# Kernel tuning notes

Measured on AMD Instinct MI355X. Metric: run time of the kernel, lower is better.

Reference implementation:

```python
import jax, jax.numpy as jnp
import numpy as np

B, T, D_IN, D_OUT = 4, 2048, 1024, 1024


def setup_inputs() -> dict:
    key = jax.random.key(0)
    k1, k2, k3, k4 = jax.random.split(key, 4)
    s_in = 1.0 / np.sqrt(D_IN)
    return {
        "input_vector": jax.random.normal(k1, (B, T, D_IN), dtype=jnp.float32),
        "w_q": jax.random.normal(k2, (D_IN, D_OUT), dtype=jnp.float32) * s_in,
        "w_k": jax.random.normal(k3, (D_IN, D_OUT), dtype=jnp.float32) * s_in,
        "w_v": jax.random.normal(k4, (D_IN, D_OUT), dtype=jnp.float32) * s_in,
    }


def reference(input_vector, w_q, w_k, w_v):
    # projections: [B, T, D_OUT]
    q = jnp.einsum("btd,de->bte", input_vector, w_q)
    k = jnp.einsum("btd,de->bte", input_vector, w_k)
    v = jnp.einsum("btd,de->bte", input_vector, w_v)

    T_ = q.shape[1]
    # raw scores [B, T, T]
    scores = jnp.einsum("bqd,bkd->bqk", q, k)
    # causal mask (strict upper triangle masked to -inf), applied BEFORE scaling
    # (as in the original; -inf is invariant under the scale anyway)
    causal = jnp.tril(jnp.ones((T_, T_), dtype=bool))  # True = keep
    scores = jnp.where(causal[None, :, :], scores, -jnp.inf)
    scores = scores / jnp.sqrt(jnp.asarray(k.shape[-1], scores.dtype))
    attn = jax.nn.softmax(scores, axis=-1)
    # dropout = 0.0 (eval): identity
    return jnp.einsum("bqk,bkd->bqd", attn, v)
```

## Files before the change

### kernel.cpp

```cpp
#include <hip/hip_runtime.h>
#include <cstdint>
#include <math.h>

typedef unsigned short u16;
typedef __attribute__((ext_vector_type(8))) short short8;
typedef __attribute__((ext_vector_type(16))) float f32x16;

__device__ __forceinline__ u16 f2bf(float f) {
  uint32_t u = __float_as_uint(f);
  u += 0x7FFFu + ((u >> 16) & 1u);
  return (u16)(u >> 16);
}
__device__ __forceinline__ float bf2f(u16 h) {
  return __uint_as_float(((uint32_t)h) << 16);
}

__device__ __forceinline__ void async_ld16(u16* lds, const u16* g) {
  __builtin_amdgcn_global_load_lds((const __attribute__((address_space(1))) uint32_t*)g,
                                   (__attribute__((address_space(3))) uint32_t*)lds,
                                   16, 0, 0);
}

template <int MODE, bool KLIM, int EPI>
__global__ __launch_bounds__(256) void gemm_bt(
    const u16* __restrict__ A, int lda, long zsA,
    const u16* __restrict__ B, int ldb, long zsB,
    void* __restrict__ Cv, int ldc, long zsC,
    float* __restrict__ l, int K, float scale, int NB)
{
  const int b = blockIdx.x, zb = blockIdx.y;
  int nb, mb;
  if constexpr (MODE == 1) {
    const int u = b & 7, v = b >> 3;
    nb = v & (NB - 1);
    mb = u * ((int)(gridDim.x >> 3) / NB) + (v / NB);
  } else if constexpr (MODE == 2) {
    const int u = b & 7, idx = b >> 3;
    if (idx <= u) { mb = u;      nb = idx; }
    else          { mb = 15 - u; nb = idx - u - 1; }
  } else if constexpr (MODE == 3) {
    const int u = b & 7, idx = b >> 3;
    mb = (idx < 8) ? u : 15 - u;
    nb = idx & 7;
  } else {
    nb = b % NB;
    mb = b / NB;
  }

  A += (long)zb * zsA;
  B += (long)zb * zsB;
  const int m0 = mb * 128, n0 = nb * 128;

  __shared__ __align__(16) u16 lsA[2][128 * 32];
  __shared__ __align__(16) u16 lsB[2][128 * 32];

  const int tid = threadIdx.x;
  const int lane = tid & 63;
  const int wave = tid >> 6;
  const int wr = (wave >> 1) * 64;
  const int wc = (wave & 1) * 64;

  f32x16 acc[2][2];
#pragma unroll
  for (int i = 0; i < 2; ++i)
#pragma unroll
    for (int j = 0; j < 2; ++j)
#pragma unroll
      for (int r = 0; r < 16; ++r) acc[i][j][r] = 0.f;

  const int c0 = tid;
  const int c1 = tid + 256;
  const int r0 = c0 >> 2, q0 = ((c0 & 3) ^ ((c0 >> 3) & 3)) * 8;
  const int r1 = c1 >> 2, q1 = ((c1 & 3) ^ ((c1 >> 3) & 3)) * 8;

  const int klim = (mb + 1) * 128;
  const int kmax = KLIM ? (K < klim ? K : klim) : K;

  const u16* pA0 = A + (long)(m0 + r0) * lda + q0;
  const u16* pA1 = A + (long)(m0 + r1) * lda + q1;
  const u16* pB0 = B + (long)(n0 + r0) * ldb + q0;
  const u16* pB1 = B + (long)(n0 + r1) * ldb + q1;

  const int m32 = lane & 31;
  const int hh = lane >> 5;
  const int rsw = (m32 >> 1) & 3;
  int offA[2][2], offB[2][2];
#pragma unroll
  for (int i = 0; i < 2; ++i)
#pragma unroll
    for (int ks = 0; ks < 2; ++ks) {
      const int kq = ((ks << 1) | hh) ^ rsw;
      offA[i][ks] = (wr + i * 32 + m32) * 32 + kq * 8;
      offB[i][ks] = (wc + i * 32 + m32) * 32 + kq * 8;
    }

  async_ld16(&lsA[0][c0 * 8], pA0);
  async_ld16(&lsA[0][c1 * 8], pA1);
  async_ld16(&lsB[0][c0 * 8], pB0);
  async_ld16(&lsB[0][c1 * 8], pB1);
  pA0 += 32; pA1 += 32; pB0 += 32; pB1 += 32;

  int p = 0;
  for (int k0 = 0; k0 < kmax; k0 += 32) {
    __syncthreads();
    if (k0 + 32 < kmax) {
      async_ld16(&lsA[p ^ 1][c0 * 8], pA0);
      async_ld16(&lsA[p ^ 1][c1 * 8], pA1);
      async_ld16(&lsB[p ^ 1][c0 * 8], pB0);
      async_ld16(&lsB[p ^ 1][c1 * 8], pB1);
      pA0 += 32; pA1 += 32; pB0 += 32; pB1 += 32;
    }

    const u16* la = lsA[p];
    const u16* lb = lsB[p];
#pragma unroll
    for (int ks = 0; ks < 2; ++ks) {
      const short8 a0 = *(const short8*)&la[offA[0][ks]];
      const short8 a1 = *(const short8*)&la[offA[1][ks]];
      const short8 b0 = *(const short8*)&lb[offB[0][ks]];
      const short8 b1 = *(const short8*)&lb[offB[1][ks]];
      acc[0][0] = __builtin_amdgcn_mfma_f32_32x32x16_bf16(a0, b0, acc[0][0], 0, 0, 0);
      acc[0][1] = __builtin_amdgcn_mfma_f32_32x32x16_bf16(a0, b1, acc[0][1], 0, 0, 0);
      acc[1][0] = __builtin_amdgcn_mfma_f32_32x32x16_bf16(a1, b0, acc[1][0], 0, 0, 0);
      acc[1][1] = __builtin_amdgcn_mfma_f32_32x32x16_bf16(a1, b1, acc[1][1], 0, 0, 0);
    }
    p ^= 1;
  }

  const int ec = lane & 31;
  const int rb = (lane >> 5) * 4;

  if constexpr (EPI == 1) {
    u16* C = (u16*)Cv + (long)zb * zsC;
#pragma unroll
    for (int i = 0; i < 2; ++i) {
      const int rbase = m0 + wr + i * 32 + rb;
#pragma unroll
      for (int j = 0; j < 2; ++j) {
        const int col = n0 + wc + j * 32 + ec;
#pragma unroll
        for (int r = 0; r < 16; ++r) {
          const int row = rbase + (r & 3) + 8 * (r >> 2);
          C[(long)row * ldc + col] = f2bf(acc[i][j][r] * scale);
        }
      }
    }
  } else if constexpr (EPI == 2) {
    u16* C = (u16*)Cv + (long)zb * zsC;
    float* lz = l + (long)zb * 2048;
#pragma unroll
    for (int i = 0; i < 2; ++i) {
      const int rbase = m0 + wr + i * 32 + rb;
      float rsum[16];
#pragma unroll
      for (int r = 0; r < 16; ++r) rsum[r] = 0.f;
#pragma unroll
      for (int j = 0; j < 2; ++j) {
        const int col = n0 + wc + j * 32 + ec;
#pragma unroll
        for (int r = 0; r < 16; ++r) {
          const int row = rbase + (r & 3) + 8 * (r >> 2);
          float pv = __expf(acc[i][j][r] * scale);
          if (col > row) pv = 0.f;
          C[(long)row * ldc + col] = f2bf(pv);
          rsum[r] += pv;
        }
      }
#pragma unroll
      for (int r = 0; r < 16; ++r) {
        float s = rsum[r];
#pragma unroll
        for (int off = 1; off < 32; off <<= 1) s += __shfl_xor(s, off, 64);
        if ((lane & 31) == 0)
          atomicAdd(&lz[rbase + (r & 3) + 8 * (r >> 2)], s);
      }
    }
  } else {
    float* C = (float*)Cv + (long)zb * zsC;
    const float* lz = l + (long)zb * 2048;
#pragma unroll
    for (int i = 0; i < 2; ++i) {
      const int rbase = m0 + wr + i * 32 + rb;
#pragma unroll
      for (int j = 0; j < 2; ++j) {
        const int col = n0 + wc + j * 32 + ec;
#pragma unroll
        for (int r = 0; r < 16; ++r) {
          const int row = rbase + (r & 3) + 8 * (r >> 2);
          C[(long)row * ldc + col] = acc[i][j][r] / lz[row];
        }
      }
    }
  }
}

__global__ __launch_bounds__(256) void cast_x_kernel(const float* __restrict__ x,
                                                     u16* __restrict__ y,
                                                     float* __restrict__ l) {
  const long i = ((long)blockIdx.x * 256 + threadIdx.x) * 4;
  const float4 v = *(const float4*)(x + i);
  ushort4 o;
  o.x = f2bf(v.x); o.y = f2bf(v.y); o.z = f2bf(v.z); o.w = f2bf(v.w);
  *(ushort4*)(y + i) = o;
  if (blockIdx.x == 0) {
    float4 z = {0.f, 0.f, 0.f, 0.f};
#pragma unroll
    for (int k = 0; k < 8; ++k)
      ((float4*)l)[threadIdx.x * 8 + k] = z;
  }
}

__global__ __launch_bounds__(256) void cast_wt_kernel(const float* __restrict__ w0,
                                                      const float* __restrict__ w1,
                                                      const float* __restrict__ w2,
                                                      u16* __restrict__ Wt) {
  const float* W = (blockIdx.z == 0) ? w0 : (blockIdx.z == 1) ? w1 : w2;
  u16* o = Wt + (long)blockIdx.z * 1024 * 1024;
  __shared__ float t[32][33];
  const int n0 = blockIdx.x * 32, k0 = blockIdx.y * 32;
  const int tx = threadIdx.x, ty = threadIdx.y;
  for (int r = ty; r < 32; r += 8) t[r][tx] = W[(long)(k0 + r) * 1024 + n0 + tx];
  __syncthreads();
  for (int r = ty; r < 32; r += 8) o[(long)(n0 + r) * 1024 + k0 + tx] = f2bf(t[tx][r]);
}

__global__ __launch_bounds__(256) void transpose_v_kernel(const u16* __restrict__ V,
                                                          u16* __restrict__ Vt) {
  __shared__ u16 t[32][33];
  const int d0 = blockIdx.x * 32, t0 = blockIdx.y * 32, b = blockIdx.z;
  const u16* Vb = V + (long)b * 2048 * 1024;
  u16* Ob = Vt + (long)b * 1024 * 2048;
  const int tx = threadIdx.x, ty = threadIdx.y;
  for (int r = ty; r < 32; r += 8) t[r][tx] = Vb[(long)(t0 + r) * 1024 + d0 + tx];
  __syncthreads();
  for (int r = ty; r < 32; r += 8) Ob[(long)(d0 + r) * 2048 + t0 + tx] = t[tx][r];
}

extern "C" void kernel_launch(void* const* d_in, const int* in_sizes, int n_in,
                              void* d_out, int out_size, void* d_ws, size_t ws_size,
                              hipStream_t stream) {
  const float* X  = (const float*)d_in[0];
  const float* Wq = (const float*)d_in[1];
  const float* Wk = (const float*)d_in[2];
  const float* Wv = (const float*)d_in[3];
  float* out = (float*)d_out;

  const long BT = 8192;
  const long Tq = 2048, D = 1024;

  u16* Xbf = (u16*)d_ws;
  u16* Wt  = Xbf + BT * D;
  u16* QKV = Wt + 3 * D * D;
  u16* Vt  = QKV + 3 * BT * D;
  u16* P   = Vt + 4 * D * Tq;
  float* l = (float*)(P + 4 * Tq * Tq);

  cast_x_kernel<<<8192, 256, 0, stream>>>(X, Xbf, l);
  cast_wt_kernel<<<dim3(32, 32, 3), dim3(32, 8), 0, stream>>>(Wq, Wk, Wv, Wt);

  gemm_bt<1, false, 1><<<dim3(512, 3), 256, 0, stream>>>(
      Xbf, 1024, 0L, Wt, 1024, D * D, QKV, 1024, BT * D, nullptr, 1024, 1.0f, 8);

  gemm_bt<2, false, 2><<<dim3(136, 4), 256, 0, stream>>>(
      QKV, 1024, Tq * D, QKV + BT * D, 1024, Tq * D,
      P, 2048, Tq * Tq, l, 1024, 0.03125f, 16);

  transpose_v_kernel<<<dim3(32, 64, 4), dim3(32, 8), 0, stream>>>(QKV + 2 * BT * D, Vt);

  gemm_bt<3, true, 3><<<dim3(128, 4), 256, 0, stream>>>(
      P, 2048, Tq * Tq, Vt, 2048, D * Tq,
      out, 1024, Tq * D, l, 2048, 1.0f, 8);
}
```

Baseline: 283.6 us.

## Compute V transposed directly, fuse scores with V projection, replace atomics with partials

The V projection now runs as Wv^T·X^T, so V is produced already transposed and the separate transpose kernel goes away. That projection is also merged into the same launch as the causal score/exp kernel. Row sums are written as per-column-block partials instead of atomicAdds, which also removes the zeroing of l. The PV kernel reduces those partials into shared memory before normalizing. The two cast kernels are merged into one launch, for fewer launches and less memory traffic overall, at the cost of a more complex role-dispatch kernel and strided Vt writes.

```diff
diff --git a/kernel.cpp b/kernel.cpp
--- a/kernel.cpp
+++ b/kernel.cpp
@@ -1,6 +1,5 @@
 #include <hip/hip_runtime.h>
 #include <cstdint>
-#include <math.h>
 
 typedef unsigned short u16;
 typedef __attribute__((ext_vector_type(8))) short short8;
@@ -11,9 +10,6 @@
   u += 0x7FFFu + ((u >> 16) & 1u);
   return (u16)(u >> 16);
 }
-__device__ __forceinline__ float bf2f(u16 h) {
-  return __uint_as_float(((uint32_t)h) << 16);
-}
 
 __device__ __forceinline__ void async_ld16(u16* lds, const u16* g) {
   __builtin_amdgcn_global_load_lds((const __attribute__((address_space(1))) uint32_t*)g,
@@ -21,98 +17,119 @@
                                    16, 0, 0);
 }
 
-template <int MODE, bool KLIM, int EPI>
-__global__ __launch_bounds__(256) void gemm_bt(
-    const u16* __restrict__ A, int lda, long zsA,
-    const u16* __restrict__ B, int ldb, long zsB,
-    void* __restrict__ Cv, int ldc, long zsC,
-    float* __restrict__ l, int K, float scale, int NB)
+template <int ROLE>
+__global__ __launch_bounds__(256) void gk(
+    const u16* __restrict__ Xbf, const u16* __restrict__ Wt,
+    u16* __restrict__ QK, u16* __restrict__ VtAll,
+    u16* __restrict__ P, float* __restrict__ lpart,
+    float* __restrict__ out)
 {
-  const int b = blockIdx.x, zb = blockIdx.y;
-  int nb, mb;
-  if constexpr (MODE == 1) {
-    const int u = b & 7, v = b >> 3;
-    nb = v & (NB - 1);
-    mb = u * ((int)(gridDim.x >> 3) / NB) + (v / NB);
-  } else if constexpr (MODE == 2) {
-    const int u = b & 7, idx = b >> 3;
-    if (idx <= u) { mb = u;      nb = idx; }
-    else          { mb = 15 - u; nb = idx - u - 1; }
-  } else if constexpr (MODE == 3) {
-    const int u = b & 7, idx = b >> 3;
-    mb = (idx < 8) ? u : 15 - u;
-    nb = idx & 7;
-  } else {
-    nb = b % NB;
-    mb = b / NB;
-  }
-
-  A += (long)zb * zsA;
-  B += (long)zb * zsB;
-  const int m0 = mb * 128, n0 = nb * 128;
-
-  __shared__ __align__(16) u16 lsA[2][128 * 32];
-  __shared__ __align__(16) u16 lsB[2][128 * 32];
-
+  const int b = blockIdx.x;
   const int tid = threadIdx.x;
   const int lane = tid & 63;
   const int wave = tid >> 6;
   const int wr = (wave >> 1) * 64;
   const int wc = (wave & 1) * 64;
 
-  f32x16 acc[2][2];
-#pragma unroll
-  for (int i = 0; i < 2; ++i)
-#pragma unroll
-    for (int j = 0; j < 2; ++j)
-#pragma unroll
-      for (int r = 0; r < 16; ++r) acc[i][j][r] = 0.f;
-
-  const int c0 = tid;
-  const int c1 = tid + 256;
+  __shared__ __align__(16) u16 ls[4][4096];
+  __shared__ float l_s[128];
+
+  const int c0 = tid, c1 = tid + 256;
   const int r0 = c0 >> 2, q0 = ((c0 & 3) ^ ((c0 >> 3) & 3)) * 8;
   const int r1 = c1 >> 2, q1 = ((c1 & 3) ^ ((c1 >> 3) & 3)) * 8;
 
-  const int klim = (mb + 1) * 128;
-  const int kmax = KLIM ? (K < klim ? K : klim) : K;
+  const int m32 = lane & 31;
+  const int hh = lane >> 5;
+  const int rsw = (m32 >> 1) & 3;
+  int offA[2][2], offB[2][2];
+#pragma unroll
+  for (int i = 0; i < 2; ++i)
+#pragma unroll
+    for (int ks = 0; ks < 2; ++ks) {
+      const int kq = ((ks << 1) | hh) ^ rsw;
+      offA[i][ks] = (wr + i * 32 + m32) * 32 + kq * 8;
+      offB[i][ks] = (wc + i * 32 + m32) * 32 + kq * 8;
+    }
+
+  const u16 *A, *B;
+  int lda, ldb, kmax, m0, n0, mb, nb, zb = 0, mat = 0;
+  bool scoresRole = false;
+
+  if constexpr (ROLE == 0) {
+    const int u = b & 7, v = b >> 3;
+    mat = v >> 6;
+    const int w = v & 63;
+    nb = w & 7;
+    mb = u * 8 + (w >> 3);
+    A = Xbf; lda = 1024;
+    B = Wt + (long)mat * 1024 * 1024; ldb = 1024;
+    kmax = 1024;
+  } else if constexpr (ROLE == 1) {
+    if (b < 544) {
+      scoresRole = true;
+      const int u = b & 7, t = b >> 3;
+      zb = t / 17;
+      const int idx = t % 17;
+      if (idx <= u) { mb = u;      nb = idx; }
+      else          { mb = 15 - u; nb = idx - u - 1; }
+      A = QK + (long)zb * 2048 * 1024; lda = 1024;
+      B = QK + 8192L * 1024 + (long)zb * 2048 * 1024; ldb = 1024;
+      kmax = 1024;
+    } else {
+      const int v = b - 544;
+      const int u = v & 7, w = v >> 3;
+      mb = w & 7;
+      nb = u * 8 + (w >> 3);
+      A = Wt + 2L * 1024 * 1024; lda = 1024;
+      B = Xbf; ldb = 1024;
+      kmax = 1024;
+    }
+  } else {
+    const int u = b & 7, idx = b >> 3;
+    zb = blockIdx.y;
+    if (idx < 8) { mb = 15 - u; nb = idx; }
+    else         { mb = u;      nb = idx - 8; }
+    A = P + (long)zb * 2048 * 2048; lda = 2048;
+    B = VtAll + (long)zb * 2048; ldb = 8192;
+    kmax = (mb + 1) * 128;
+  }
+  m0 = mb * 128;
+  n0 = nb * 128;
 
   const u16* pA0 = A + (long)(m0 + r0) * lda + q0;
   const u16* pA1 = A + (long)(m0 + r1) * lda + q1;
   const u16* pB0 = B + (long)(n0 + r0) * ldb + q0;
   const u16* pB1 = B + (long)(n0 + r1) * ldb + q1;
 
-  const int m32 = lane & 31;
-  const int hh = lane >> 5;
-  const int rsw = (m32 >> 1) & 3;
-  int offA[2][2], offB[2][2];
+  f32x16 acc[2][2];
 #pragma unroll
   for (int i = 0; i < 2; ++i)
 #pragma unroll
-    for (int ks = 0; ks < 2; ++ks) {
-      const int kq = ((ks << 1) | hh) ^ rsw;
-      offA[i][ks] = (wr + i * 32 + m32) * 32 + kq * 8;
-      offB[i][ks] = (wc + i * 32 + m32) * 32 + kq * 8;
-    }
-
-  async_ld16(&lsA[0][c0 * 8], pA0);
-  async_ld16(&lsA[0][c1 * 8], pA1);
-  async_ld16(&lsB[0][c0 * 8], pB0);
-  async_ld16(&lsB[0][c1 * 8], pB1);
+    for (int j = 0; j < 2; ++j)
+#pragma unroll
+      for (int r = 0; r < 16; ++r) acc[i][j][r] = 0.f;
+
+  async_ld16(&ls[0][c0 * 8 - 0], pA0);
+  async_ld16(&ls[0][c1 * 8 - 2048 * 0], pA1);
+  async_ld16(&ls[2][c0 * 8], pB0);
+  async_ld16(&ls[2][c1 * 8 - 2048 * 0], pB1);
   pA0 += 32; pA1 += 32; pB0 += 32; pB1 += 32;
 
   int p = 0;
   for (int k0 = 0; k0 < kmax; k0 += 32) {
     __syncthreads();
     if (k0 + 32 < kmax) {
-      async_ld16(&lsA[p ^ 1][c0 * 8], pA0);
-      async_ld16(&lsA[p ^ 1][c1 * 8], pA1);
-      async_ld16(&lsB[p ^ 1][c0 * 8], pB0);
-      async_ld16(&lsB[p ^ 1][c1 * 8], pB1);
+      u16* la = ls[p ^ 1];
+      u16* lb = ls[2 + (p ^ 1)];
+      async_ld16(&la[c0 * 8], pA0);
+      async_ld16(&la[c1 * 8], pA1);
+      async_ld16(&lb[c0 * 8], pB0);
+      async_ld16(&lb[c1 * 8], pB1);
       pA0 += 32; pA1 += 32; pB0 += 32; pB1 += 32;
     }
 
-    const u16* la = lsA[p];
-    const u16* lb = lsB[p];
+    const u16* la = ls[p];
+    const u16* lb = ls[2 + p];
 #pragma unroll
     for (int ks = 0; ks < 2; ++ks) {
       const short8 a0 = *(const short8*)&la[offA[0][ks]];
@@ -130,8 +147,8 @@
   const int ec = lane & 31;
   const int rb = (lane >> 5) * 4;
 
-  if constexpr (EPI == 1) {
-    u16* C = (u16*)Cv + (long)zb * zsC;
+  if constexpr (ROLE == 0) {
+    u16* C = QK + (long)mat * 8192 * 1024;
 #pragma unroll
     for (int i = 0; i < 2; ++i) {
       const int rbase = m0 + wr + i * 32 + rb;
@@ -141,99 +158,110 @@
 #pragma unroll
         for (int r = 0; r < 16; ++r) {
           const int row = rbase + (r & 3) + 8 * (r >> 2);
-          C[(long)row * ldc + col] = f2bf(acc[i][j][r] * scale);
-        }
-      }
-    }
-  } else if constexpr (EPI == 2) {
-    u16* C = (u16*)Cv + (long)zb * zsC;
-    float* lz = l + (long)zb * 2048;
+          C[(long)row * 1024 + col] = f2bf(acc[i][j][r]);
+        }
+      }
+    }
+  } else if constexpr (ROLE == 1) {
+    if (scoresRole) {
+      u16* C = P + (long)zb * 2048 * 2048;
+      float* lp = lpart + (long)zb * 32 * 2048 + (long)(2 * nb + (wc >> 6)) * 2048;
+#pragma unroll
+      for (int i = 0; i < 2; ++i) {
+        const int rbl = wr + i * 32 + rb;
+        float rsum[16];
+#pragma unroll
+        for (int r = 0; r < 16; ++r) rsum[r] = 0.f;
+#pragma unroll
+        for (int j = 0; j < 2; ++j) {
+          const int col = n0 + wc + j * 32 + ec;
+#pragma unroll
+          for (int r = 0; r < 16; ++r) {
+            const int row = m0 + rbl + (r & 3) + 8 * (r >> 2);
+            float pv = __expf(acc[i][j][r] * 0.03125f);
+            if (col > row) pv = 0.f;
+            C[(long)row * 2048 + col] = f2bf(pv);
+            rsum[r] += pv;
+          }
+        }
+#pragma unroll
+        for (int r = 0; r < 16; ++r) {
+          float s = rsum[r];
+#pragma unroll
+          for (int off = 1; off < 32; off <<= 1) s += __shfl_xor(s, off, 64);
+          if ((lane & 31) == 0)
+            lp[m0 + rbl + (r & 3) + 8 * (r >> 2)] = s;
+        }
+      }
+    } else {
+#pragma unroll
+      for (int i = 0; i < 2; ++i) {
+        const int rbase = m0 + wr + i * 32 + rb;
+#pragma unroll
+        for (int j = 0; j < 2; ++j) {
+          const int col = n0 + wc + j * 32 + ec;
+#pragma unroll
+          for (int r = 0; r < 16; ++r) {
+            const int row = rbase + (r & 3) + 8 * (r >> 2);
+            VtAll[(long)row * 8192 + col] = f2bf(acc[i][j][r]);
+          }
+        }
+      }
+    }
+  } else {
+    __syncthreads();
+    if (tid < 128) {
+      const float* lp = lpart + (long)zb * 32 * 2048 + m0 + tid;
+      float s0 = 0.f, s1 = 0.f;
+      const int nch = 2 * (mb + 1);
+      for (int c = 0; c < nch; c += 2) {
+        s0 += lp[(long)c * 2048];
+        s1 += lp[(long)(c + 1) * 2048];
+      }
+      l_s[tid] = 1.f / (s0 + s1);
+    }
+    __syncthreads();
+    float* C = out + (long)zb * 2048 * 1024;
 #pragma unroll
     for (int i = 0; i < 2; ++i) {
-      const int rbase = m0 + wr + i * 32 + rb;
-      float rsum[16];
-#pragma unroll
-      for (int r = 0; r < 16; ++r) rsum[r] = 0.f;
+      const int rbl = wr + i * 32 + rb;
 #pragma unroll
       for (int j = 0; j < 2; ++j) {
         const int col = n0 + wc + j * 32 + ec;
 #pragma unroll
         for (int r = 0; r < 16; ++r) {
-          const int row = rbase + (r & 3) + 8 * (r >> 2);
-          float pv = __expf(acc[i][j][r] * scale);
-          if (col > row) pv = 0.f;
-          C[(long)row * ldc + col] = f2bf(pv);
-          rsum[r] += pv;
-        }
-      }
-#pragma unroll
-      for (int r = 0; r < 16; ++r) {
-        float s = rsum[r];
-#pragma unroll
-        for (int off = 1; off < 32; off <<= 1) s += __shfl_xor(s, off, 64);
-        if ((lane & 31) == 0)
-          atomicAdd(&lz[rbase + (r & 3) + 8 * (r >> 2)], s);
-      }
-    }
+          const int rl = rbl + (r & 3) + 8 * (r >> 2);
+          C[(long)(m0 + rl) * 1024 + col] = acc[i][j][r] * l_s[rl];
+        }
+      }
+    }
+  }
+}
+
+__global__ __launch_bounds__(256) void cast_fused(
+    const float* __restrict__ x, const float* __restrict__ w0,
+    const float* __restrict__ w1, const float* __restrict__ w2,
+    u16* __restrict__ Xbf, u16* __restrict__ Wt)
+{
+  const int b = blockIdx.x;
+  if (b < 8192) {
+    const long i = ((long)b * 256 + threadIdx.x) * 4;
+    const float4 v = *(const float4*)(x + i);
+    ushort4 o;
+    o.x = f2bf(v.x); o.y = f2bf(v.y); o.z = f2bf(v.z); o.w = f2bf(v.w);
+    *(ushort4*)(Xbf + i) = o;
   } else {
-    float* C = (float*)Cv + (long)zb * zsC;
-    const float* lz = l + (long)zb * 2048;
-#pragma unroll
-    for (int i = 0; i < 2; ++i) {
-      const int rbase = m0 + wr + i * 32 + rb;
-#pragma unroll
-      for (int j = 0; j < 2; ++j) {
-        const int col = n0 + wc + j * 32 + ec;
-#pragma unroll
-        for (int r = 0; r < 16; ++r) {
-          const int row = rbase + (r & 3) + 8 * (r >> 2);
-          C[(long)row * ldc + col] = acc[i][j][r] / lz[row];
-        }
-      }
-    }
-  }
-}
-
-__global__ __launch_bounds__(256) void cast_x_kernel(const float* __restrict__ x,
-                                                     u16* __restrict__ y,
-                                                     float* __restrict__ l) {
-  const long i = ((long)blockIdx.x * 256 + threadIdx.x) * 4;
-  const float4 v = *(const float4*)(x + i);
-  ushort4 o;
-  o.x = f2bf(v.x); o.y = f2bf(v.y); o.z = f2bf(v.z); o.w = f2bf(v.w);
-  *(ushort4*)(y + i) = o;
-  if (blockIdx.x == 0) {
-    float4 z = {0.f, 0.f, 0.f, 0.f};
-#pragma unroll
-    for (int k = 0; k < 8; ++k)
-      ((float4*)l)[threadIdx.x * 8 + k] = z;
-  }
-}
-
-__global__ __launch_bounds__(256) void cast_wt_kernel(const float* __restrict__ w0,
-                                                      const float* __restrict__ w1,
-                                                      const float* __restrict__ w2,
-                                                      u16* __restrict__ Wt) {
-  const float* W = (blockIdx.z == 0) ? w0 : (blockIdx.z == 1) ? w1 : w2;
-  u16* o = Wt + (long)blockIdx.z * 1024 * 1024;
-  __shared__ float t[32][33];
-  const int n0 = blockIdx.x * 32, k0 = blockIdx.y * 32;
-  const int tx = threadIdx.x, ty = threadIdx.y;
-  for (int r = ty; r < 32; r += 8) t[r][tx] = W[(long)(k0 + r) * 1024 + n0 + tx];
-  __syncthreads();
-  for (int r = ty; r < 32; r += 8) o[(long)(n0 + r) * 1024 + k0 + tx] = f2bf(t[tx][r]);
-}
-
-__global__ __launch_bounds__(256) void transpose_v_kernel(const u16* __restrict__ V,
-                                                          u16* __restrict__ Vt) {
-  __shared__ u16 t[32][33];
-  const int d0 = blockIdx.x * 32, t0 = blockIdx.y * 32, b = blockIdx.z;
-  const u16* Vb = V + (long)b * 2048 * 1024;
-  u16* Ob = Vt + (long)b * 1024 * 2048;
-  const int tx = threadIdx.x, ty = threadIdx.y;
-  for (int r = ty; r < 32; r += 8) t[r][tx] = Vb[(long)(t0 + r) * 1024 + d0 + tx];
-  __syncthreads();
-  for (int r = ty; r < 32; r += 8) Ob[(long)(d0 + r) * 2048 + t0 + tx] = t[tx][r];
+    const int bb = b - 8192;
+    const int z = bb >> 10, rem = bb & 1023;
+    const float* W = (z == 0) ? w0 : (z == 1) ? w1 : w2;
+    u16* o = Wt + (long)z * 1024 * 1024;
+    __shared__ float t[32][33];
+    const int n0 = (rem & 31) * 32, k0 = (rem >> 5) * 32;
+    const int tx = threadIdx.x & 31, ty = threadIdx.x >> 5;
+    for (int r = ty; r < 32; r += 8) t[r][tx] = W[(long)(k0 + r) * 1024 + n0 + tx];
+    __syncthreads();
+    for (int r = ty; r < 32; r += 8) o[(long)(n0 + r) * 1024 + k0 + tx] = f2bf(t[tx][r]);
+  }
 }
 
 extern "C" void kernel_launch(void* const* d_in, const int* in_sizes, int n_in,
@@ -245,29 +273,18 @@
   const float* Wv = (const float*)d_in[3];
   float* out = (float*)d_out;
 
-  const long BT = 8192;
-  const long Tq = 2048, D = 1024;
-
-  u16* Xbf = (u16*)d_ws;
-  u16* Wt  = Xbf + BT * D;
-  u16* QKV = Wt + 3 * D * D;
-  u16* Vt  = QKV + 3 * BT * D;
-  u16* P   = Vt + 4 * D * Tq;
-  float* l = (float*)(P + 4 * Tq * Tq);
-
-  cast_x_kernel<<<8192, 256, 0, stream>>>(X, Xbf, l);
-  cast_wt_kernel<<<dim3(32, 32, 3), dim3(32, 8), 0, stream>>>(Wq, Wk, Wv, Wt);
-
-  gemm_bt<1, false, 1><<<dim3(512, 3), 256, 0, stream>>>(
-      Xbf, 1024, 0L, Wt, 1024, D * D, QKV, 1024, BT * D, nullptr, 1024, 1.0f, 8);
-
-  gemm_bt<2, false, 2><<<dim3(136, 4), 256, 0, stream>>>(
-      QKV, 1024, Tq * D, QKV + BT * D, 1024, Tq * D,
-      P, 2048, Tq * Tq, l, 1024, 0.03125f, 16);
-
-  transpose_v_kernel<<<dim3(32, 64, 4), dim3(32, 8), 0, stream>>>(QKV + 2 * BT * D, Vt);
-
-  gemm_bt<3, true, 3><<<dim3(128, 4), 256, 0, stream>>>(
-      P, 2048, Tq * Tq, Vt, 2048, D * Tq,
-      out, 1024, Tq * D, l, 2048, 1.0f, 8);
-}
+  u16* Xbf   = (u16*)d_ws;
+  u16* Wt    = Xbf + 8192L * 1024;
+  u16* QK    = Wt + 3L * 1024 * 1024;
+  u16* VtAll = QK + 2L * 8192 * 1024;
+  u16* P     = VtAll + 1024L * 8192;
+  float* lpart = (float*)(P + 4L * 2048 * 2048);
+
+  cast_fused<<<8192 + 3072, 256, 0, stream>>>(X, Wq, Wk, Wv, Xbf, Wt);
+
+  gk<0><<<1024, 256, 0, stream>>>(Xbf, Wt, QK, VtAll, P, lpart, out);
+
+  gk<1><<<1056, 256, 0, stream>>>(Xbf, Wt, QK, VtAll, P, lpart, out);
+
+  gk<2><<<dim3(128, 4), 256, 0, stream>>>(Xbf, Wt, QK, VtAll, P, lpart, out);
+}
```

New measurement: 253.0 us. 10.8% less time.
